# Optimization experiments

Measured on AMD Instinct MI355X. Metric: run time of the kernel, lower is better.

The kernel has to match this reference:

```python
import jax, jax.numpy as jnp
import numpy as np

EPS = 1e-5
NUM_SUBSET = 3

def conv1x1(x, w, b):
    # x: (N,C,T,V), w: (O,C), b: (O,)
    return jnp.einsum('nctv,oc->notv', x, w) + b[None, :, None, None]

def batchnorm(x, w, b):
    m = x.mean(axis=(0, 2, 3), keepdims=True)
    v = x.var(axis=(0, 2, 3), keepdims=True)
    return (x - m) * jax.lax.rsqrt(v + EPS) * w[None, :, None, None] + b[None, :, None, None]

def setup_inputs() -> dict:
    key = jax.random.key(0)
    ks = jax.random.split(key, 16)
    N, C, T, V, R, O, S = 32, 64, 256, 25, 8, 64, NUM_SUBSET
    sc = 0.05
    return {
        'x1': jax.random.normal(ks[0], (N, C, T, V), jnp.float32),
        'x2': jax.random.normal(ks[1], (N, C, T, V), jnp.float32),
        'PA': jax.random.normal(ks[2], (S, V, V), jnp.float32) * sc,
        'alpha': jnp.zeros((1,), jnp.float32),
        'c1w': jax.random.normal(ks[3], (S, R, C), jnp.float32) * sc,
        'c1b': jnp.zeros((S, R), jnp.float32),
        'c2w': jax.random.normal(ks[4], (S, R, C), jnp.float32) * sc,
        'c2b': jnp.zeros((S, R), jnp.float32),
        'c3w': jax.random.normal(ks[5], (S, O, C), jnp.float32) * sc,
        'c3b': jnp.zeros((S, O), jnp.float32),
        'c4w': jax.random.normal(ks[6], (S, O, C), jnp.float32) * sc,
        'c4b': jnp.zeros((S, O), jnp.float32),
        'c5w': jax.random.normal(ks[7], (S, O, R), jnp.float32) * sc,
        'c5b': jnp.zeros((S, O), jnp.float32),
        'c6w': jax.random.normal(ks[8], (S, O, R), jnp.float32) * sc,
        'c6b': jnp.zeros((S, O), jnp.float32),
        'bn1_w': jax.random.uniform(ks[9], (O,), jnp.float32),
        'bn1_b': jnp.zeros((O,), jnp.float32),
        'bn2_w': jax.random.uniform(ks[10], (O,), jnp.float32),
        'bn2_b': jnp.zeros((O,), jnp.float32),
    }

def reference(x1, x2, PA, alpha, c1w, c1b, c2w, c2b, c3w, c3b, c4w, c4b,
              c5w, c5b, c6w, c6b, bn1_w, bn1_b, bn2_w, bn2_b):
    y1 = y2 = None
    for i in range(NUM_SUBSET):
        r1 = conv1x1(x1, c1w[i], c1b[i]).mean(axis=2)  # (N,R,V)
        r2 = conv1x1(x2, c2w[i], c2b[i]).mean(axis=2)  # (N,R,V)
        x3 = conv1x1(x1, c3w[i], c3b[i])               # (N,O,T,V)
        x4 = conv1x1(x2, c4w[i], c4b[i])               # (N,O,T,V)
        rel = jnp.tanh(r1[:, :, :, None] - r2[:, :, None, :])  # (N,R,V,V)
        # NOTE: source passes self.alpha (scalar param) into the A2 slot,
        # so the `alpha` multiplier on conv5 defaults to 1.
        a1 = jnp.einsum('nruv,or->nouv', rel, c5w[i]) + c5b[i][None, :, None, None]
        a1 = a1 + PA[i][None, None, :, :]
        a2 = jnp.einsum('nruv,or->nouv', rel, c6w[i]) + c6b[i][None, :, None, None] + alpha
        z1 = jnp.einsum('ncuv,nctv->nctu', a1, x3)
        z2 = jnp.einsum('ncuv,nctv->nctu', a2, x4)
        y1 = z1 if y1 is None else y1 + z1
        y2 = z2 if y2 is None else y2 + z2
    # in_channels == out_channels -> residual down is identity
    y1 = jax.nn.relu(batchnorm(y1, bn1_w, bn1_b) + x1)
    y2 = jax.nn.relu(batchnorm(y2, bn2_w, bn2_b) + x2)
    return (y1, y2)
```

## Files before the change

### kernel.cpp

```cpp
#include <hip/hip_runtime.h>
#include <hip/hip_bf16.h>

typedef float  f32x4  __attribute__((ext_vector_type(4)));
typedef short  bf16x8 __attribute__((ext_vector_type(8)));
typedef short  s16x4  __attribute__((ext_vector_type(4)));

__device__ __forceinline__ unsigned short f2bf(float f) {
    __hip_bfloat16 h = __float2bfloat16(f);
    return *reinterpret_cast<unsigned short*>(&h);
}
__device__ __forceinline__ unsigned int f2bf2(float a, float b) {
    __hip_bfloat162 h = __float22bfloat162_rn(make_float2(a, b));
    return *reinterpret_cast<unsigned int*>(&h);
}
__device__ __forceinline__ unsigned short f2bf_bit(float f) {
    unsigned int u = __float_as_uint(f);
    unsigned int r = (u + 0x7FFFu + ((u >> 16) & 1u)) >> 16;
    return (unsigned short)r;
}
__device__ __forceinline__ float bf2f(unsigned short h) {
    return __uint_as_float(((unsigned int)h) << 16);
}

__global__ __launch_bounds__(256) void kT_transpose(
    const float* __restrict__ x1, const float* __restrict__ x2,
    float* __restrict__ xmp, unsigned short* __restrict__ xT)
{
    const int tc = blockIdx.x, n = blockIdx.y, p = blockIdx.z;
    const float* __restrict__ x = p ? x2 : x1;
    __shared__ unsigned short tile[64 * 226];
    const int tid = threadIdx.x;

    const size_t xb = (size_t)n * 409600 + (size_t)tc * 200;
    for (int k = 0; k < 13; k++) {
        const int idx = tid + k * 256;
        if (idx < 3200) {
            const int c = idx / 50, l = idx % 50;
            const f32x4 v = *(const f32x4*)(x + xb + (size_t)c * 6400 + l * 4);
            unsigned int* dst = (unsigned int*)&tile[c * 226 + l * 4];
            dst[0] = f2bf2(v[0], v[1]);
            dst[1] = f2bf2(v[2], v[3]);
        }
    }
    __syncthreads();

    for (int k = 0; k < 7; k++) {
        const int idx = tid + k * 256;
        if (idx < 1600) {
            const int c = idx / 25, v = idx % 25;
            float s = 0.f;
            #pragma unroll
            for (int t = 0; t < 8; t++) s += bf2f(tile[c * 226 + t * 25 + v]);
            xmp[((size_t)((p * 32 + n) * 32 + tc)) * 1600 + idx] =
                s * (1.0f / 256.0f);
        }
    }

    for (int k = 0; k < 7; k++) {
        const int idx = tid + k * 256;
        if (idx < 1600) {
            const int c8 = idx & 7, pos = idx >> 3;
            bf16x8 o;
            #pragma unroll
            for (int j = 0; j < 8; j++)
                o[j] = (short)tile[(c8 * 8 + j) * 226 + pos];
            *(bf16x8*)(xT + (((size_t)(p * 32 + n) * 6400 + tc * 200 + pos) * 64
                             + c8 * 8)) = o;
        }
    }
}

__global__ void k2_adj(const float* __restrict__ xmp,
                       const float* __restrict__ PA, const float* __restrict__ alpha,
                       const float* __restrict__ c1w, const float* __restrict__ c1b,
                       const float* __restrict__ c2w, const float* __restrict__ c2b,
                       const float* __restrict__ c5w, const float* __restrict__ c5b,
                       const float* __restrict__ c6w, const float* __restrict__ c6b,
                       unsigned short* __restrict__ aw,
                       const float* __restrict__ c3w, const float* __restrict__ c4w,
                       unsigned short* __restrict__ awW)
{
    const int b = blockIdx.x;
    const int tid = threadIdx.x;

    if (b >= 192) {
        const int pi = b - 192;
        const int p = pi / 3, i = pi % 3;
        const int cg = tid >> 6, lane = tid & 63, q = lane >> 4, m = lane & 15;
        const float* w3 = p ? c4w : c3w;
        const float* wr = w3 + (size_t)(i * 64 + cg * 16 + m) * 64 + q * 8;
        const f32x4 w00 = *(const f32x4*)(wr);
        const f32x4 w01 = *(const f32x4*)(wr + 4);
        const f32x4 w10 = *(const f32x4*)(wr + 32);
        const f32x4 w11 = *(const f32x4*)(wr + 36);
        bf16x8 af0, af1;
        #pragma unroll
        for (int k = 0; k < 4; k++) {
            af0[k] = (short)f2bf(w00[k]); af0[k + 4] = (short)f2bf(w01[k]);
            af1[k] = (short)f2bf(w10[k]); af1[k + 4] = (short)f2bf(w11[k]);
        }
        unsigned short* o = awW + ((size_t)(pi * 4 + cg) * 64 + lane) * 16;
        *(bf16x8*)(o)     = af0;
        *(bf16x8*)(o + 8) = af1;
        return;
    }

    const int i = b >> 6;
    const int n = (b >> 1) & 31;
    const int pp = b & 1;
    __shared__ float xml[3200];
    __shared__ float rl[400];
    __shared__ float rel[5000];

    for (int idx = tid; idx < 800; idx += 256) {
        const int p_ = idx / 400, r4 = (idx % 400) * 4;
        f32x4 s = (f32x4){0.f, 0.f, 0.f, 0.f};
        #pragma unroll 4
        for (int tcc = 0; tcc < 32; tcc++)
            s += *(const f32x4*)(xmp + ((size_t)((p_ * 32 + n) * 32 + tcc)) * 1600 + r4);
        *(f32x4*)(xml + p_ * 1600 + r4) = s;
    }
    __syncthreads();

    for (int idx = tid; idx < 400; idx += 256) {
        const int which = idx / 200;
        const int rr = (idx % 200) / 25;
        const int v = idx % 25;
        const float* wv = (which ? c2w : c1w) + (i * 8 + rr) * 64;
        const float* xp = xml + which * 1600;
        float s = (which ? c2b : c1b)[i * 8 + rr];
        for (int c = 0; c < 64; c++) s += wv[c] * xp[c * 25 + v];
        rl[idx] = s;
    }
    __syncthreads();

    for (int idx = tid; idx < 5000; idx += 256) {
        const int r_ = idx / 625;
        const int rem = idx - r_ * 625;
        const int u = rem / 25;
        const int v = rem - u * 25;
        rel[idx] = tanhf(rl[r_ * 25 + u] - rl[200 + r_ * 25 + v]);
    }
    __syncthreads();

    const float al = alpha[0];
    {
        const int p_ = pp;
        const float* w5 = p_ ? c6w : c5w;
        const float* b5 = p_ ? c6b : c5b;
        for (int idx = tid; idx < 8192; idx += 256) {
            const int c = idx >> 7;
            const int ut = (idx >> 6) & 1;
            const int lane = idx & 63;
            const int u = ut * 16 + (lane & 15);
            const int qd = lane >> 4;
            bf16x8 outv;
            if (u < 25) {
                float wrow[8];
                #pragma unroll
                for (int r = 0; r < 8; r++) wrow[r] = w5[(i * 64 + c) * 8 + r];
                const float bias = b5[i * 64 + c];
                #pragma unroll
                for (int j = 0; j < 8; j++) {
                    const int v = qd * 8 + j;
                    float s = 0.f;
                    if (v < 25) {
                        s = bias + (p_ ? al : PA[i * 625 + u * 25 + v]);
                        #pragma unroll
                        for (int r = 0; r < 8; r++) s += rel[r * 625 + u * 25 + v] * wrow[r];
                    }
                    outv[j] = (short)f2bf(s);
                }
            } else {
                #pragma unroll
                for (int j = 0; j < 8; j++) outv[j] = 0;
            }
            *(bf16x8*)(aw + ((size_t)((p_ * 3 + i) * 32 + n) * 64 + c) * 1024
                          + ut * 512 + lane * 8) = outv;
        }
    }
}

__global__ __launch_bounds__(256, 3) void kF_main(
    const unsigned short* __restrict__ xT,
    const float* __restrict__ c3b, const float* __restrict__ c4b,
    const unsigned short* __restrict__ awW,
    const unsigned short* __restrict__ aw,
    unsigned short* __restrict__ z,
    float* __restrict__ ppart)
{
    const int flat = blockIdx.x;
    const int lidx = flat >> 3;
    const int grp  = (flat & 7) * 8 + (lidx >> 6);
    const int within = lidx & 63;
    const int tc = within & 15, cg = within >> 4;
    const int n = grp & 31, p = grp >> 5;

    __shared__ unsigned short X3s[2][16 * 512];
    const int tid = threadIdx.x, w = tid >> 6, lane = tid & 63;
    const int q = lane >> 4, m = lane & 15;

    {
        int* xi = (int*)&X3s[0][0];
        #pragma unroll
        for (int k = 0; k < 32; k++) xi[tid + k * 256] = 0;
    }

    const float* __restrict__ b3 = p ? c4b : c3b;
    const size_t xTb = ((size_t)(p * 32 + n) * 6400 + (size_t)tc * 400) * 64;

    bf16x8 xr0[7], xr1[7];
    #pragma unroll
    for (int k = 0; k < 7; k++) {
        const int g = w + 4 * k;
        if (g < 25) {
            const unsigned short* xp = xT + xTb + (size_t)(g * 16 + m) * 64 + q * 8;
            xr0[k] = *(const bf16x8*)(xp);
            xr1[k] = *(const bf16x8*)(xp + 32);
        }
    }

    f32x4 acc[4][2];
    #pragma unroll
    for (int a = 0; a < 4; a++) {
        acc[a][0] = (f32x4){0.f, 0.f, 0.f, 0.f};
        acc[a][1] = (f32x4){0.f, 0.f, 0.f, 0.f};
    }

    __syncthreads();

    for (int i = 0; i < 3; i++) {
        bf16x8 B0[4], B1[4];
        #pragma unroll
        for (int cl4 = 0; cl4 < 4; cl4++) {
            const int c = cg * 16 + w * 4 + cl4;
            const unsigned short* ab =
                aw + ((size_t)((p * 3 + i) * 32 + n) * 64 + c) * 1024 + lane * 8;
            B0[cl4] = *(const bf16x8*)(ab);
            B1[cl4] = *(const bf16x8*)(ab + 512);
        }

        const unsigned short* wp =
            awW + ((size_t)((p * 3 + i) * 4 + cg) * 64 + lane) * 16;
        const bf16x8 af0 = *(const bf16x8*)(wp);
        const bf16x8 af1 = *(const bf16x8*)(wp + 8);
        float bb[4];
        #pragma unroll
        for (int r = 0; r < 4; r++) bb[r] = b3[i * 64 + cg * 16 + q * 4 + r];

        unsigned short* Xb = &X3s[i & 1][0];
        #pragma unroll
        for (int k = 0; k < 7; k++) {
            const int g = w + 4 * k;
            if (g < 25) {
                f32x4 d = (f32x4){0.f, 0.f, 0.f, 0.f};
                d = __builtin_amdgcn_mfma_f32_16x16x32_bf16(af0, xr0[k], d, 0, 0, 0);
                d = __builtin_amdgcn_mfma_f32_16x16x32_bf16(af1, xr1[k], d, 0, 0, 0);
                const int pos = g * 16 + m;
                const int t = pos / 25, v = pos - t * 25;
                #pragma unroll
                for (int r = 0; r < 4; r++)
                    Xb[(q * 4 + r) * 512 + t * 32 + v] = f2bf_bit(d[r] + bb[r]);
            }
        }
        __syncthreads();

        #pragma unroll
        for (int cl4 = 0; cl4 < 4; cl4++) {
            const int cl = w * 4 + cl4;
            const bf16x8 A = *(const bf16x8*)(Xb + cl * 512 + m * 32 + q * 8);
            acc[cl4][0] = __builtin_amdgcn_mfma_f32_16x16x32_bf16(A, B0[cl4], acc[cl4][0], 0, 0, 0);
            acc[cl4][1] = __builtin_amdgcn_mfma_f32_16x16x32_bf16(A, B1[cl4], acc[cl4][1], 0, 0, 0);
        }
    }
    __syncthreads();

    unsigned short* stg = &X3s[0][0];
    #pragma unroll
    for (int cl4 = 0; cl4 < 4; cl4++) {
        float sum = 0.f, ssq = 0.f;
        #pragma unroll
        for (int r = 0; r < 4; r++) {
            const float v0 = acc[cl4][0][r];
            sum += v0; ssq += v0 * v0;
        }
        if (m < 9) {
            #pragma unroll
            for (int r = 0; r < 4; r++) {
                const float v1 = acc[cl4][1][r];
                sum += v1; ssq += v1 * v1;
            }
        }
        #pragma unroll
        for (int off = 32; off > 0; off >>= 1) {
            sum += __shfl_xor(sum, off, 64);
            ssq += __shfl_xor(ssq, off, 64);
        }
        const int c = cg * 16 + w * 4 + cl4;
        if (lane == 0) {
            float* pp = ppart + ((size_t)(p * 64 + c) * 512 + n * 16 + tc) * 2;
            pp[0] = sum; pp[1] = ssq;
        }
        #pragma unroll
        for (int ut = 0; ut < 2; ut++) {
            if (ut == 0 || m < 9) {
                #pragma unroll
                for (int r = 0; r < 4; r++)
                    stg[w * 1600 + cl4 * 400 + (q * 4 + r) * 25 + ut * 16 + m] =
                        f2bf_bit(acc[cl4][ut][r]);
            }
        }
    }
    for (int rd = 0; rd < 4; rd++) {
        const int idx = rd * 64 + lane;
        if (idx < 200) {
            const int cl4 = idx / 50, oct = idx % 50;
            const bf16x8 vz = *(const bf16x8*)(stg + w * 1600 + cl4 * 400 + oct * 8);
            const int c = cg * 16 + w * 4 + cl4;
            *(bf16x8*)(z + ((size_t)((p * 32 + n) * 64 + c)) * 6400
                         + tc * 400 + oct * 8) = vz;
        }
    }
}

__global__ void k4_finalize(const float* __restrict__ ppart,
                            const float* __restrict__ bn1w, const float* __restrict__ bn1b,
                            const float* __restrict__ bn2w, const float* __restrict__ bn2b,
                            float* __restrict__ ss)
{
    const int b = blockIdx.x;
    const int t = threadIdx.x;
    const float* base = ppart + (size_t)b * 1024;
    float s = 0.f, qs = 0.f;
    #pragma unroll
    for (int k = 0; k < 8; k++) {
        const int idx = t + 64 * k;
        s  += base[idx * 2];
        qs += base[idx * 2 + 1];
    }
    #pragma unroll
    for (int off = 32; off > 0; off >>= 1) {
        s  += __shfl_xor(s,  off, 64);
        qs += __shfl_xor(qs, off, 64);
    }
    if (t == 0) {
        const int p = b >> 6, c = b & 63;
        const float cnt = 204800.f;
        const float mean = s / cnt;
        const float var  = qs / cnt - mean * mean;
        const float gw = p ? bn2w[c] : bn1w[c];
        const float gb = p ? bn2b[c] : bn1b[c];
        const float scale = gw * rsqrtf(var + 1e-5f);
        ss[b * 2]     = scale;
        ss[b * 2 + 1] = gb - mean * scale;
    }
}

__global__ __launch_bounds__(256) void k5_apply(
    const float* __restrict__ x1, const float* __restrict__ x2,
    const unsigned short* __restrict__ z, const float* __restrict__ ss,
    float* __restrict__ out)
{
    const unsigned int g = blockIdx.x * 256u + threadIdx.x;
    const unsigned int e = g * 4u;
    const int p = (e >= 13107200u) ? 1 : 0;
    const unsigned int c = (e / 6400u) & 63u;
    const float* xsrc = p ? x2 : x1;
    const f32x4 xv = *(const f32x4*)(xsrc + (e - (unsigned int)p * 13107200u));
    const s16x4 zv = *(const s16x4*)(const void*)(z + e);
    const float scale = ss[(p * 64 + c) * 2];
    const float shift = ss[(p * 64 + c) * 2 + 1];
    f32x4 o;
    #pragma unroll
    for (int k = 0; k < 4; k++) {
        const float zf = bf2f((unsigned short)zv[k]);
        const float y = zf * scale + shift + xv[k];
        o[k] = y > 0.f ? y : 0.f;
    }
    *(f32x4*)(out + e) = o;
}

extern "C" void kernel_launch(void* const* d_in, const int* in_sizes, int n_in,
                              void* d_out, int out_size, void* d_ws, size_t ws_size,
                              hipStream_t stream)
{
    (void)in_sizes; (void)n_in; (void)out_size; (void)ws_size;
    const float* x1   = (const float*)d_in[0];
    const float* x2   = (const float*)d_in[1];
    const float* PA   = (const float*)d_in[2];
    const float* alp  = (const float*)d_in[3];
    const float* c1w  = (const float*)d_in[4];
    const float* c1b  = (const float*)d_in[5];
    const float* c2w  = (const float*)d_in[6];
    const float* c2b  = (const float*)d_in[7];
    const float* c3w  = (const float*)d_in[8];
    const float* c3b  = (const float*)d_in[9];
    const float* c4w  = (const float*)d_in[10];
    const float* c4b  = (const float*)d_in[11];
    const float* c5w  = (const float*)d_in[12];
    const float* c5b  = (const float*)d_in[13];
    const float* c6w  = (const float*)d_in[14];
    const float* c6b  = (const float*)d_in[15];
    const float* bn1w = (const float*)d_in[16];
    const float* bn1b = (const float*)d_in[17];
    const float* bn2w = (const float*)d_in[18];
    const float* bn2b = (const float*)d_in[19];

    char* ws = (char*)d_ws;
    unsigned short* aw    = (unsigned short*)(ws + 0);
    unsigned short* xT    = (unsigned short*)(ws + 25165824);
    unsigned short* zbuf  = (unsigned short*)(ws + 77594624);
    float*          ppart = (float*)(ws + 130023424);
    float*          ss    = (float*)(ws + 130547712);
    unsigned short* awW   = (unsigned short*)(ws + 130548736);
    float*          xmp   = (float*)zbuf;

    kT_transpose<<<dim3(32, 32, 2), 256, 0, stream>>>(x1, x2, xmp, xT);
    k2_adj<<<198, 256, 0, stream>>>(xmp, PA, alp, c1w, c1b, c2w, c2b,
                                    c5w, c5b, c6w, c6b, aw, c3w, c4w, awW);
    kF_main<<<dim3(4096), 256, 0, stream>>>(xT, c3b, c4b, awW, aw,
                                            zbuf, ppart);
    k4_finalize<<<128, 64, 0, stream>>>(ppart, bn1w, bn1b, bn2w, bn2b, ss);
    k5_apply<<<25600, 256, 0, stream>>>(x1, x2, zbuf, ss, (float*)d_out);
}
```

Measured before the change: 380.4 us.

## Split adjacency kernel into rel computation and wide packing kernels

```diff
diff --git a/kernel.cpp b/kernel.cpp
--- a/kernel.cpp
+++ b/kernel.cpp
@@ -70,21 +70,19 @@
     }
 }
 
-__global__ void k2_adj(const float* __restrict__ xmp,
-                       const float* __restrict__ PA, const float* __restrict__ alpha,
-                       const float* __restrict__ c1w, const float* __restrict__ c1b,
-                       const float* __restrict__ c2w, const float* __restrict__ c2b,
-                       const float* __restrict__ c5w, const float* __restrict__ c5b,
-                       const float* __restrict__ c6w, const float* __restrict__ c6b,
-                       unsigned short* __restrict__ aw,
-                       const float* __restrict__ c3w, const float* __restrict__ c4w,
-                       unsigned short* __restrict__ awW)
+__global__ __launch_bounds__(256) void k2a_rel(
+    const float* __restrict__ xmp,
+    const float* __restrict__ c1w, const float* __restrict__ c1b,
+    const float* __restrict__ c2w, const float* __restrict__ c2b,
+    float* __restrict__ relg,
+    const float* __restrict__ c3w, const float* __restrict__ c4w,
+    unsigned short* __restrict__ awW)
 {
     const int b = blockIdx.x;
     const int tid = threadIdx.x;
 
-    if (b >= 192) {
-        const int pi = b - 192;
+    if (b >= 96) {
+        const int pi = b - 96;
         const int p = pi / 3, i = pi % 3;
         const int cg = tid >> 6, lane = tid & 63, q = lane >> 4, m = lane & 15;
         const float* w3 = p ? c4w : c3w;
@@ -105,12 +103,9 @@
         return;
     }
 
-    const int i = b >> 6;
-    const int n = (b >> 1) & 31;
-    const int pp = b & 1;
+    const int i = b >> 5, n = b & 31;
     __shared__ float xml[3200];
     __shared__ float rl[400];
-    __shared__ float rel[5000];
 
     for (int idx = tid; idx < 800; idx += 256) {
         const int p_ = idx / 400, r4 = (idx % 400) * 4;
@@ -139,45 +134,68 @@
         const int rem = idx - r_ * 625;
         const int u = rem / 25;
         const int v = rem - u * 25;
-        rel[idx] = tanhf(rl[r_ * 25 + u] - rl[200 + r_ * 25 + v]);
-    }
+        relg[(size_t)b * 5024 + idx] =
+            tanhf(rl[r_ * 25 + u] - rl[200 + r_ * 25 + v]);
+    }
+}
+
+__global__ __launch_bounds__(256) void k2b_pack(
+    const float* __restrict__ relg,
+    const float* __restrict__ PA, const float* __restrict__ alpha,
+    const float* __restrict__ c5w, const float* __restrict__ c5b,
+    const float* __restrict__ c6w, const float* __restrict__ c6b,
+    unsigned short* __restrict__ aw)
+{
+    const int b = blockIdx.x;
+    const int cq = b & 7;
+    const int pp = (b >> 3) & 1;
+    const int n  = (b >> 4) & 31;
+    const int i  = b >> 9;
+    const int tid = threadIdx.x;
+
+    __shared__ float rel[5000];
+    const float* rsrc = relg + (size_t)(i * 32 + n) * 5024;
+    for (int idx = tid; idx < 1250; idx += 256)
+        *(f32x4*)(&rel[idx * 4]) = *(const f32x4*)(rsrc + idx * 4);
     __syncthreads();
 
     const float al = alpha[0];
-    {
-        const int p_ = pp;
-        const float* w5 = p_ ? c6w : c5w;
-        const float* b5 = p_ ? c6b : c5b;
-        for (int idx = tid; idx < 8192; idx += 256) {
-            const int c = idx >> 7;
-            const int ut = (idx >> 6) & 1;
-            const int lane = idx & 63;
-            const int u = ut * 16 + (lane & 15);
-            const int qd = lane >> 4;
-            bf16x8 outv;
-            if (u < 25) {
-                float wrow[8];
-                #pragma unroll
-                for (int r = 0; r < 8; r++) wrow[r] = w5[(i * 64 + c) * 8 + r];
-                const float bias = b5[i * 64 + c];
-                #pragma unroll
-                for (int j = 0; j < 8; j++) {
-                    const int v = qd * 8 + j;
-                    float s = 0.f;
-                    if (v < 25) {
-                        s = bias + (p_ ? al : PA[i * 625 + u * 25 + v]);
-                        #pragma unroll
-                        for (int r = 0; r < 8; r++) s += rel[r * 625 + u * 25 + v] * wrow[r];
-                    }
-                    outv[j] = (short)f2bf(s);
+    const float* w5 = pp ? c6w : c5w;
+    const float* b5 = pp ? c6b : c5b;
+
+    #pragma unroll
+    for (int k = 0; k < 4; k++) {
+        const int item = tid + k * 256;
+        const int cc = item >> 7;
+        const int c  = cq * 8 + cc;
+        const int ut = (item >> 6) & 1;
+        const int lane = item & 63;
+        const int u = ut * 16 + (lane & 15);
+        const int qd = lane >> 4;
+        bf16x8 outv;
+        if (u < 25) {
+            float wrow[8];
+            #pragma unroll
+            for (int r = 0; r < 8; r++) wrow[r] = w5[(i * 64 + c) * 8 + r];
+            const float bias = b5[i * 64 + c];
+            #pragma unroll
+            for (int j = 0; j < 8; j++) {
+                const int v = qd * 8 + j;
+                float s = 0.f;
+                if (v < 25) {
+                    s = bias + (pp ? al : PA[i * 625 + u * 25 + v]);
+                    #pragma unroll
+                    for (int r = 0; r < 8; r++)
+                        s += rel[r * 625 + u * 25 + v] * wrow[r];
                 }
-            } else {
-                #pragma unroll
-                for (int j = 0; j < 8; j++) outv[j] = 0;
+                outv[j] = (short)f2bf(s);
             }
-            *(bf16x8*)(aw + ((size_t)((p_ * 3 + i) * 32 + n) * 64 + c) * 1024
-                          + ut * 512 + lane * 8) = outv;
-        }
+        } else {
+            #pragma unroll
+            for (int j = 0; j < 8; j++) outv[j] = 0;
+        }
+        *(bf16x8*)(aw + ((size_t)((pp * 3 + i) * 32 + n) * 64 + c) * 1024
+                      + ut * 512 + lane * 8) = outv;
     }
 }
 
@@ -414,10 +432,12 @@
     float*          ss    = (float*)(ws + 130547712);
     unsigned short* awW   = (unsigned short*)(ws + 130548736);
     float*          xmp   = (float*)zbuf;
+    float*          relg  = (float*)(ws + 77594624 + 13107200);
 
     kT_transpose<<<dim3(32, 32, 2), 256, 0, stream>>>(x1, x2, xmp, xT);
-    k2_adj<<<198, 256, 0, stream>>>(xmp, PA, alp, c1w, c1b, c2w, c2b,
-                                    c5w, c5b, c6w, c6b, aw, c3w, c4w, awW);
+    k2a_rel<<<102, 256, 0, stream>>>(xmp, c1w, c1b, c2w, c2b, relg,
+                                     c3w, c4w, awW);
+    k2b_pack<<<1536, 256, 0, stream>>>(relg, PA, alp, c5w, c5b, c6w, c6b, aw);
     kF_main<<<dim3(4096), 256, 0, stream>>>(xT, c3b, c4b, awW, aw,
                                             zbuf, ppart);
     k4_finalize<<<128, 64, 0, stream>>>(ppart, bn1w, bn1b, bn2w, bn2b, ss);
```

Result: faster. 353.9 us (-7.0%).
